# Kernel optimization log

Hardware: AMD Instinct MI355X
Metric: run time of the kernel (lower is better)

## Reference

```python
import jax, jax.numpy as jnp
import numpy as np

N = 50000          # total nodes (types: 20000/17000/13000)
E = 800000         # edges, avg degree 16
NUM_ETYPES = 6
ALPHA = 0.05       # residual-attention blend coefficient
SLOPE = 0.2        # leaky_relu negative slope


def _edge_softmax(e, dst, n):
    # softmax over incoming edges of each destination node; e: [E, H]
    m = jax.ops.segment_max(e, dst, num_segments=n)      # [N, H]
    ex = jnp.exp(e - m[dst])
    s = jax.ops.segment_sum(ex, dst, num_segments=n)     # [N, H]
    return ex / s[dst]


def _gat_layer(h, src, dst, etype, W, We, eemb, al, ar, ae, resW, res_attn, activate):
    n = h.shape[0]
    H, out = al.shape
    feat = (h @ W).reshape(n, H, out)                    # [N, H, out]
    T, edim = eemb.shape
    # edge-type attention term: embedding -> fc_e -> attn_e; only T distinct rows
    et_att = jnp.einsum('thd,hd->th', (eemb @ We).reshape(T, H, edim), ae)  # [T, H]
    el = jnp.einsum('nho,ho->nh', feat, al)              # [N, H]
    er = jnp.einsum('nho,ho->nh', feat, ar)              # [N, H]
    e = jax.nn.leaky_relu(el[src] + er[dst] + et_att[etype], SLOPE)  # [E, H]
    a = _edge_softmax(e, dst, n)                         # [E, H]
    if res_attn is not None:
        a = a * (1.0 - ALPHA) + res_attn * ALPHA
    rst = jax.ops.segment_sum(feat[src] * a[:, :, None], dst, num_segments=n)  # [N, H, out]
    if resW is not None:
        rst = rst + (h @ resW).reshape(n, H, out)
    if activate:
        rst = jax.nn.elu(rst)
    return rst, jax.lax.stop_gradient(a)


def _forward(x0, x1, x2, fcw0, fcb0, fcw1, fcb1, fcw2, fcb2,
             W0, We0, eemb0, al0, ar0, ae0,
             W1, We1, eemb1, al1, ar1, ae1, resW1,
             W2, We2, eemb2, al2, ar2, ae2, resW2,
             src, dst, etype):
    # per-type input projection then concat (feat_drop=0 -> identity)
    h = jnp.concatenate([x0 @ fcw0 + fcb0, x1 @ fcw1 + fcb1, x2 @ fcw2 + fcb2], axis=0)  # [N, 64]
    h1, a = _gat_layer(h, src, dst, etype, W0, We0, eemb0, al0, ar0, ae0, None, None, True)
    h1 = h1.reshape(h1.shape[0], -1)                     # [N, 256]
    h2, a = _gat_layer(h1, src, dst, etype, W1, We1, eemb1, al1, ar1, ae1, resW1, a, True)
    h2 = h2.reshape(h2.shape[0], -1)                     # [N, 256]
    logits, _ = _gat_layer(h2, src, dst, etype, W2, We2, eemb2, al2, ar2, ae2, resW2, None, False)
    return logits                                        # [N, 1, 16]


def setup_inputs():
    key = jax.random.key(0)
    ks = iter(jax.random.split(key, 48))
    def rn(shape, fan_in):
        return jax.random.normal(next(ks), shape, jnp.float32) / np.sqrt(fan_in)
    inp = {}
    inp['x0'] = jax.random.normal(next(ks), (20000, 128), jnp.float32)
    inp['x1'] = jax.random.normal(next(ks), (17000, 256), jnp.float32)
    inp['x2'] = jax.random.normal(next(ks), (13000, 64), jnp.float32)
    inp['fcw0'] = rn((128, 64), 128); inp['fcb0'] = jnp.zeros((64,), jnp.float32)
    inp['fcw1'] = rn((256, 64), 256); inp['fcb1'] = jnp.zeros((64,), jnp.float32)
    inp['fcw2'] = rn((64, 64), 64);   inp['fcb2'] = jnp.zeros((64,), jnp.float32)
    # layer 0: in=64 -> H=8, out=32
    inp['W0'] = rn((64, 256), 64); inp['We0'] = rn((64, 512), 64)
    inp['eemb0'] = rn((NUM_ETYPES, 64), 1.0)
    inp['al0'] = rn((8, 32), 32); inp['ar0'] = rn((8, 32), 32); inp['ae0'] = rn((8, 64), 64)
    # layer 1: in=256 -> H=8, out=32, residual
    inp['W1'] = rn((256, 256), 256); inp['We1'] = rn((64, 512), 64)
    inp['eemb1'] = rn((NUM_ETYPES, 64), 1.0)
    inp['al1'] = rn((8, 32), 32); inp['ar1'] = rn((8, 32), 32); inp['ae1'] = rn((8, 64), 64)
    inp['resW1'] = rn((256, 256), 256)
    # output layer: in=256 -> H=1, out=16, residual
    inp['W2'] = rn((256, 16), 256); inp['We2'] = rn((64, 64), 64)
    inp['eemb2'] = rn((NUM_ETYPES, 64), 1.0)
    inp['al2'] = rn((1, 16), 16); inp['ar2'] = rn((1, 16), 16); inp['ae2'] = rn((1, 64), 64)
    inp['resW2'] = rn((256, 16), 256)
    inp['src'] = jax.random.randint(next(ks), (E,), 0, N)
    inp['dst'] = jax.random.randint(next(ks), (E,), 0, N)
    inp['etype'] = jax.random.randint(next(ks), (E,), 0, NUM_ETYPES)
    return inp


def reference(x0, x1, x2, fcw0, fcb0, fcw1, fcb1, fcw2, fcb2,
              W0, We0, eemb0, al0, ar0, ae0,
              W1, We1, eemb1, al1, ar1, ae1, resW1,
              W2, We2, eemb2, al2, ar2, ae2, resW2,
              src, dst, etype):
    return _forward(x0, x1, x2, fcw0, fcb0, fcw1, fcb1, fcw2, fcb2,
                    W0, We0, eemb0, al0, ar0, ae0,
                    W1, We1, eemb1, al1, ar1, ae1, resW1,
                    W2, We2, eemb2, al2, ar2, ae2, resW2,
                    src, dst, etype)
```

## Files before the change

kernel.cpp:

```cpp
#include <hip/hip_runtime.h>
#include <hip/hip_bf16.h>

#define ALPHA 0.05f
#define SLOPE 0.2f
#define LCAP 128

typedef __attribute__((ext_vector_type(8))) short short8v;
typedef __attribute__((ext_vector_type(8))) unsigned short ushort8v;
typedef __attribute__((ext_vector_type(4))) float floatx4;

__device__ inline ushort f2b(float f) {
    uint u = __float_as_uint(f);
    return (ushort)((u + 0x7fffu + ((u >> 16) & 1u)) >> 16);
}
__device__ inline float b2f(ushort b) { return __uint_as_float(((uint)b) << 16); }

__device__ inline void gload_lds16(const ushort* g, ushort* l) {
    __builtin_amdgcn_global_load_lds(
        (const __attribute__((address_space(1))) uint*)g,
        (__attribute__((address_space(3))) uint*)l, 16, 0, 0);
}


__global__ void hist_kernel(const int* __restrict__ dst, int* __restrict__ counts, int E) {
    int e = blockIdx.x * blockDim.x + threadIdx.x;
    if (e < E) atomicAdd(&counts[dst[e]], 1);
}

__global__ __launch_bounds__(256) void scan_part(const int* __restrict__ counts,
                                                 int* __restrict__ offsets,
                                                 int* __restrict__ partial, int n) {
    __shared__ int sd[256];
    int i = blockIdx.x * 256 + threadIdx.x;
    int v = (i < n) ? counts[i] : 0;
    sd[threadIdx.x] = v;
    __syncthreads();
    for (int off = 1; off < 256; off <<= 1) {
        int t = (threadIdx.x >= off) ? sd[threadIdx.x - off] : 0;
        __syncthreads();
        sd[threadIdx.x] += t;
        __syncthreads();
    }
    if (i < n) offsets[i + 1] = sd[threadIdx.x];
    if (threadIdx.x == 255) partial[blockIdx.x] = sd[255];
}

__global__ __launch_bounds__(256) void scan_top(int* __restrict__ partial, int nb) {
    __shared__ int sd[256];
    int v = (threadIdx.x < nb) ? partial[threadIdx.x] : 0;
    sd[threadIdx.x] = v;
    __syncthreads();
    for (int off = 1; off < 256; off <<= 1) {
        int t = (threadIdx.x >= off) ? sd[threadIdx.x - off] : 0;
        __syncthreads();
        sd[threadIdx.x] += t;
        __syncthreads();
    }
    if (threadIdx.x < nb) partial[threadIdx.x] = sd[threadIdx.x];
}

__global__ __launch_bounds__(256) void scan_add(int* __restrict__ offsets,
                                                int* __restrict__ cursor,
                                                const int* __restrict__ partial, int n) {
    int i = blockIdx.x * 256 + threadIdx.x;
    if (i >= n) return;
    int add = (blockIdx.x > 0) ? partial[blockIdx.x - 1] : 0;
    int v = offsets[i + 1] + add;
    offsets[i + 1] = v;
    if (i + 1 < n) cursor[i + 1] = v;
    if (i == 0) { offsets[0] = 0; cursor[0] = 0; }
}

__global__ void scatter_kernel(const int* __restrict__ src, const int* __restrict__ dst,
                               const int* __restrict__ et, int* __restrict__ cursor,
                               int* __restrict__ se, int E) {
    int e = blockIdx.x * blockDim.x + threadIdx.x;
    if (e >= E) return;
    int d = dst[e];
    int pos = atomicAdd(&cursor[d], 1);
    se[pos] = (src[e] << 3) | et[e];
}


__global__ void wprep3(const float* __restrict__ W0f, const float* __restrict__ W1f,
                       const float* __restrict__ WRf, ushort* __restrict__ Wt0,
                       ushort* __restrict__ Wt1, ushort* __restrict__ WtR) {
    int i = blockIdx.x * blockDim.x + threadIdx.x;
    if (i < 16384) {
        int k = i / 256, n = i % 256;
        Wt0[n * 64 + k] = f2b(W0f[i]);
    } else if (i < 16384 + 65536) {
        int j = i - 16384;
        int k = j / 256, n = j % 256;
        Wt1[n * 256 + k] = f2b(W1f[j]);
    } else if (i < 16384 + 2 * 65536) {
        int j = i - 16384 - 65536;
        int k = j / 256, n = j % 256;
        WtR[n * 256 + k] = f2b(WRf[j]);
    }
}


__global__ __launch_bounds__(512) void etype_all(
    const float* __restrict__ eemb0, const float* __restrict__ We0, const float* __restrict__ ae0, float* __restrict__ out0,
    const float* __restrict__ eemb1, const float* __restrict__ We1, const float* __restrict__ ae1, float* __restrict__ out1,
    const float* __restrict__ eemb2, const float* __restrict__ We2, const float* __restrict__ ae2, float* __restrict__ out2) {
    int layer = blockIdx.x / 6, t = blockIdx.x % 6;
    const float *eemb, *We, *ae;
    float* out;
    int H;
    if (layer == 0)      { eemb = eemb0; We = We0; ae = ae0; out = out0; H = 8; }
    else if (layer == 1) { eemb = eemb1; We = We1; ae = ae1; out = out1; H = 8; }
    else                 { eemb = eemb2; We = We2; ae = ae2; out = out2; H = 1; }
    __shared__ float es[64];
    int j = threadIdx.x;
    if (j < 64) es[j] = eemb[t * 64 + j];
    __syncthreads();
    if (j >= H * 64) return;
    float wsum = 0.f;
#pragma unroll 8
    for (int k = 0; k < 64; ++k) wsum += es[k] * We[k * (H * 64) + j];
    float v = wsum * ae[j];
#pragma unroll
    for (int off = 32; off > 0; off >>= 1) v += __shfl_down(v, off, 64);
    if ((j & 63) == 0) out[t * H + (j >> 6)] = v;
}


template<bool ATTN>
__global__ __launch_bounds__(256) void gemm_bf16(const ushort* __restrict__ A,
                                                 const ushort* __restrict__ Bt,
                                                 ushort* __restrict__ Cb,
                                                 const float* __restrict__ al,
                                                 const float* __restrict__ ar,
                                                 float* __restrict__ el,
                                                 float* __restrict__ er,
                                                 int M, int N, int K) {
    __shared__ ushort As[128 * 32];
    __shared__ ushort Bs[128 * 32];
    int bm = blockIdx.y * 128, bn = blockIdx.x * 128;
    int tid = threadIdx.x;
    int wave = tid >> 6, lane = tid & 63;
    int wm = (wave >> 1) * 64, wn = (wave & 1) * 64;
    int r = tid >> 2, c = (tid & 3) * 8;
    floatx4 acc[4][4] = {};
    for (int k0 = 0; k0 < K; k0 += 32) {
        gload_lds16(&A[(long)(bm + r) * K + k0 + c],       &As[(size_t)tid * 8]);
        gload_lds16(&A[(long)(bm + 64 + r) * K + k0 + c],  &As[(size_t)(256 + tid) * 8]);
        gload_lds16(&Bt[(long)(bn + r) * K + k0 + c],      &Bs[(size_t)tid * 8]);
        gload_lds16(&Bt[(long)(bn + 64 + r) * K + k0 + c], &Bs[(size_t)(256 + tid) * 8]);
        __syncthreads();
        int lr = lane & 15, lk = (lane >> 4) * 8;
        short8v af[4], bfr[4];
#pragma unroll
        for (int i = 0; i < 4; ++i)
            af[i] = *reinterpret_cast<const short8v*>(&As[(wm + i * 16 + lr) * 32 + lk]);
#pragma unroll
        for (int j = 0; j < 4; ++j)
            bfr[j] = *reinterpret_cast<const short8v*>(&Bs[(wn + j * 16 + lr) * 32 + lk]);
#pragma unroll
        for (int i = 0; i < 4; ++i)
#pragma unroll
            for (int j = 0; j < 4; ++j)
                acc[i][j] = __builtin_amdgcn_mfma_f32_16x16x32_bf16(af[i], bfr[j], acc[i][j], 0, 0, 0);
        __syncthreads();
    }
    int col = lane & 15, rbase = (lane >> 4) * 4;
#pragma unroll
    for (int i = 0; i < 4; ++i) {
#pragma unroll
        for (int rr = 0; rr < 4; ++rr) {
            int gm = bm + wm + i * 16 + rbase + rr;
            if (gm >= M) continue;
#pragma unroll
            for (int j = 0; j < 4; ++j) {
                int gn = bn + wn + j * 16 + col;
                Cb[(long)gm * N + gn] = f2b(acc[i][j][rr]);
            }
        }
    }
    if (ATTN) {
        int hA = (bn + wn) >> 5;
        float alv[4], arv[4];
#pragma unroll
        for (int j = 0; j < 4; ++j) {
            int h = hA + (j >> 1);
            int o = (j & 1) * 16 + col;
            alv[j] = al[h * 32 + o];
            arv[j] = ar[h * 32 + o];
        }
#pragma unroll
        for (int i = 0; i < 4; ++i) {
#pragma unroll
            for (int rr = 0; rr < 4; ++rr) {
                float slA = acc[i][0][rr] * alv[0] + acc[i][1][rr] * alv[1];
                float slB = acc[i][2][rr] * alv[2] + acc[i][3][rr] * alv[3];
                float srA = acc[i][0][rr] * arv[0] + acc[i][1][rr] * arv[1];
                float srB = acc[i][2][rr] * arv[2] + acc[i][3][rr] * arv[3];
#pragma unroll
                for (int off = 1; off < 16; off <<= 1) {
                    slA += __shfl_xor(slA, off, 64);
                    slB += __shfl_xor(slB, off, 64);
                    srA += __shfl_xor(srA, off, 64);
                    srB += __shfl_xor(srB, off, 64);
                }
                int gm = bm + wm + i * 16 + rbase + rr;
                if (col == 0 && gm < M) {
                    el[gm * 8 + hA]     = slA;
                    el[gm * 8 + hA + 1] = slB;
                    er[gm * 8 + hA]     = srA;
                    er[gm * 8 + hA + 1] = srB;
                }
            }
        }
    }
}


__global__ __launch_bounds__(256) void gemm_dual(const ushort* __restrict__ A,
                                                 const ushort* __restrict__ B1,
                                                 const ushort* __restrict__ B2,
                                                 ushort* __restrict__ C1,
                                                 ushort* __restrict__ C2,
                                                 const float* __restrict__ al,
                                                 const float* __restrict__ ar,
                                                 float* __restrict__ el,
                                                 float* __restrict__ er,
                                                 int M, int N, int K) {
    __shared__ ushort As[128 * 32];
    __shared__ ushort Bs1[128 * 32];
    __shared__ ushort Bs2[128 * 32];
    int bm = blockIdx.y * 128, bn = blockIdx.x * 128;
    int tid = threadIdx.x;
    int wave = tid >> 6, lane = tid & 63;
    int wm = (wave >> 1) * 64, wn = (wave & 1) * 64;
    int r = tid >> 2, c = (tid & 3) * 8;
    floatx4 acc1[4][4] = {};
    floatx4 acc2[4][4] = {};
    for (int k0 = 0; k0 < K; k0 += 32) {
        gload_lds16(&A[(long)(bm + r) * K + k0 + c],        &As[(size_t)tid * 8]);
        gload_lds16(&A[(long)(bm + 64 + r) * K + k0 + c],   &As[(size_t)(256 + tid) * 8]);
        gload_lds16(&B1[(long)(bn + r) * K + k0 + c],       &Bs1[(size_t)tid * 8]);
        gload_lds16(&B1[(long)(bn + 64 + r) * K + k0 + c],  &Bs1[(size_t)(256 + tid) * 8]);
        gload_lds16(&B2[(long)(bn + r) * K + k0 + c],       &Bs2[(size_t)tid * 8]);
        gload_lds16(&B2[(long)(bn + 64 + r) * K + k0 + c],  &Bs2[(size_t)(256 + tid) * 8]);
        __syncthreads();
        int lr = lane & 15, lk = (lane >> 4) * 8;
        short8v af[4], bfr[4];
#pragma unroll
        for (int i = 0; i < 4; ++i)
            af[i] = *reinterpret_cast<const short8v*>(&As[(wm + i * 16 + lr) * 32 + lk]);
#pragma unroll
        for (int j = 0; j < 4; ++j)
            bfr[j] = *reinterpret_cast<const short8v*>(&Bs1[(wn + j * 16 + lr) * 32 + lk]);
#pragma unroll
        for (int i = 0; i < 4; ++i)
#pragma unroll
            for (int j = 0; j < 4; ++j)
                acc1[i][j] = __builtin_amdgcn_mfma_f32_16x16x32_bf16(af[i], bfr[j], acc1[i][j], 0, 0, 0);
#pragma unroll
        for (int j = 0; j < 4; ++j)
            bfr[j] = *reinterpret_cast<const short8v*>(&Bs2[(wn + j * 16 + lr) * 32 + lk]);
#pragma unroll
        for (int i = 0; i < 4; ++i)
#pragma unroll
            for (int j = 0; j < 4; ++j)
                acc2[i][j] = __builtin_amdgcn_mfma_f32_16x16x32_bf16(af[i], bfr[j], acc2[i][j], 0, 0, 0);
        __syncthreads();
    }
    int col = lane & 15, rbase = (lane >> 4) * 4;
#pragma unroll
    for (int i = 0; i < 4; ++i) {
#pragma unroll
        for (int rr = 0; rr < 4; ++rr) {
            int gm = bm + wm + i * 16 + rbase + rr;
            if (gm >= M) continue;
#pragma unroll
            for (int j = 0; j < 4; ++j) {
                int gn = bn + wn + j * 16 + col;
                C1[(long)gm * N + gn] = f2b(acc1[i][j][rr]);
                C2[(long)gm * N + gn] = f2b(acc2[i][j][rr]);
            }
        }
    }
    int hA = (bn + wn) >> 5;
    float alv[4], arv[4];
#pragma unroll
    for (int j = 0; j < 4; ++j) {
        int h = hA + (j >> 1);
        int o = (j & 1) * 16 + col;
        alv[j] = al[h * 32 + o];
        arv[j] = ar[h * 32 + o];
    }
#pragma unroll
    for (int i = 0; i < 4; ++i) {
#pragma unroll
        for (int rr = 0; rr < 4; ++rr) {
            float slA = acc1[i][0][rr] * alv[0] + acc1[i][1][rr] * alv[1];
            float slB = acc1[i][2][rr] * alv[2] + acc1[i][3][rr] * alv[3];
            float srA = acc1[i][0][rr] * arv[0] + acc1[i][1][rr] * arv[1];
            float srB = acc1[i][2][rr] * arv[2] + acc1[i][3][rr] * arv[3];
#pragma unroll
            for (int off = 1; off < 16; off <<= 1) {
                slA += __shfl_xor(slA, off, 64);
                slB += __shfl_xor(slB, off, 64);
                srA += __shfl_xor(srA, off, 64);
                srB += __shfl_xor(srB, off, 64);
            }
            int gm = bm + wm + i * 16 + rbase + rr;
            if (col == 0 && gm < M) {
                el[gm * 8 + hA]     = slA;
                el[gm * 8 + hA + 1] = slB;
                er[gm * 8 + hA]     = srA;
                er[gm * 8 + hA + 1] = srB;
            }
        }
    }
}


__global__ __launch_bounds__(256) void matmul64_fc3(
    const float* __restrict__ A0, const float* __restrict__ A1, const float* __restrict__ A2,
    const float* __restrict__ W0, const float* __restrict__ W1, const float* __restrict__ W2,
    const float* __restrict__ b0, const float* __restrict__ b1, const float* __restrict__ b2,
    ushort* __restrict__ C, int n0, int n1, int n2) {
    int z = blockIdx.z;
    const float *A, *W, *bias;
    int M, K;
    long coff;
    if (z == 0)      { A = A0; W = W0; bias = b0; M = n0; K = 128; coff = 0; }
    else if (z == 1) { A = A1; W = W1; bias = b1; M = n1; K = 256; coff = (long)n0 * 64; }
    else             { A = A2; W = W2; bias = b2; M = n2; K = 64;  coff = (long)(n0 + n1) * 64; }
    int bm = blockIdx.y * 64;
    if (bm >= M) return;
    __shared__ float As[16][68];
    __shared__ float Bs[16][68];
    int tx = threadIdx.x % 16, ty = threadIdx.x / 16;
    float acc[4][4] = {};
    for (int k0 = 0; k0 < K; k0 += 16) {
        for (int i = threadIdx.x; i < 64 * 16; i += 256) {
            int mm = i / 16, kk = i % 16;
            int gm = bm + mm;
            As[kk][mm] = (gm < M) ? A[(long)gm * K + k0 + kk] : 0.f;
        }
        for (int i = threadIdx.x; i < 16 * 64; i += 256) {
            int kk = i / 64, nn = i % 64;
            Bs[kk][nn] = W[(long)(k0 + kk) * 64 + nn];
        }
        __syncthreads();
#pragma unroll
        for (int kk = 0; kk < 16; ++kk) {
            float a[4], b[4];
#pragma unroll
            for (int i = 0; i < 4; ++i) a[i] = As[kk][ty * 4 + i];
#pragma unroll
            for (int j = 0; j < 4; ++j) b[j] = Bs[kk][tx * 4 + j];
#pragma unroll
            for (int i = 0; i < 4; ++i)
#pragma unroll
                for (int j = 0; j < 4; ++j) acc[i][j] += a[i] * b[j];
        }
        __syncthreads();
    }
#pragma unroll
    for (int i = 0; i < 4; ++i) {
        int gm = bm + ty * 4 + i;
        if (gm >= M) continue;
#pragma unroll
        for (int j = 0; j < 4; ++j) {
            int gn = tx * 4 + j;
            C[coff + (long)gm * 64 + gn] = f2b(acc[i][j] + bias[gn]);
        }
    }
}


__global__ __launch_bounds__(256) void matmul_n16_dual(const ushort* __restrict__ A,
                                                       const float* __restrict__ W2,
                                                       const float* __restrict__ WR,
                                                       ushort* __restrict__ feat2b,
                                                       float* __restrict__ resout,
                                                       const float* __restrict__ al,
                                                       const float* __restrict__ ar,
                                                       float* __restrict__ el,
                                                       float* __restrict__ er, int M) {
    __shared__ float Ws2[256 * 16];
    __shared__ float WsR[256 * 16];
    for (int i = threadIdx.x; i < 256 * 16; i += 256) {
        Ws2[i] = W2[i];
        WsR[i] = WR[i];
    }
    __syncthreads();
    int nn = threadIdx.x % 16;
    float alv = al[nn], arv = ar[nn];
#pragma unroll
    for (int rb = 0; rb < 2; ++rb) {
        int m = blockIdx.x * 32 + rb * 16 + threadIdx.x / 16;
        if (m >= M) continue;
        float s1 = 0.f, s2 = 0.f;
        for (int k8 = 0; k8 < 32; ++k8) {
            uint4 v = *reinterpret_cast<const uint4*>(&A[(long)m * 256 + k8 * 8]);
            const uint* vp = reinterpret_cast<const uint*>(&v);
#pragma unroll
            for (int q = 0; q < 4; ++q) {
                uint w2 = vp[q];
                float f0 = __uint_as_float((w2 & 0xffffu) << 16);
                float f1 = __uint_as_float(w2 & 0xffff0000u);
                int k = k8 * 8 + q * 2;
                s1 += f0 * Ws2[(k + 0) * 16 + nn] + f1 * Ws2[(k + 1) * 16 + nn];
                s2 += f0 * WsR[(k + 0) * 16 + nn] + f1 * WsR[(k + 1) * 16 + nn];
            }
        }
        feat2b[(long)m * 16 + nn] = f2b(s1);
        resout[(long)m * 16 + nn] = s2;
        float sl = s1 * alv, sr = s1 * arv;
#pragma unroll
        for (int off = 1; off < 16; off <<= 1) {
            sl += __shfl_xor(sl, off, 64);
            sr += __shfl_xor(sr, off, 64);
        }
        if (nn == 0) { el[m] = sl; er[m] = sr; }
    }
}


template<bool BLEND, bool SAVE, bool RES>
__global__ __launch_bounds__(64) void fused_edge_h8(
    const int* __restrict__ offsets, const int* __restrict__ se,
    const float* __restrict__ el, const float* __restrict__ er,
    const float* __restrict__ etatt,
    const ushort* __restrict__ featb,
    const ushort* __restrict__ a0_in, ushort* __restrict__ a0_out,
    const ushort* __restrict__ resin, ushort* __restrict__ outb, int N) {
    int d = blockIdx.x;
    int lane = threadIdx.x;
    int lo = offsets[d], hi = offsets[d + 1];
    int deg = hi - lo;
    __shared__ float a_lds[LCAP][8];
    __shared__ int   s_lds[LCAP];
    __shared__ float er_s[8];
    __shared__ float m_s[8], inv_s[8];
    if (lane < 8) er_s[lane] = er[d * 8 + lane];
    __syncthreads();
    bool fast = (deg <= LCAP);
    int half = lane >> 5, t = lane & 31;
    int h8 = t >> 2;
    uint4 pf[4];
    int npf = 0;
    if (fast) {
        for (int i = lane; i < deg * 8; i += 64) {
            int p = i >> 3, h = i & 7;
            int v0 = se[lo + p];
            int s = v0 >> 3, tt = v0 & 7;
            if (h == 0) s_lds[p] = s;
            float v = el[s * 8 + h] + er_s[h] + etatt[tt * 8 + h];
            a_lds[p][h] = v > 0.f ? v : SLOPE * v;
        }
        __syncthreads();
#pragma unroll
        for (int u = 0; u < 4; ++u) {
            int p = half + 2 * u;
            if (p < deg) {
                pf[u] = *reinterpret_cast<const uint4*>(&featb[(long)s_lds[p] * 256 + t * 8]);
                npf = u + 1;
            }
        }
        {
            int g = lane >> 3, h = lane & 7;
            float m = -INFINITY;
            for (int p = g; p < deg; p += 8) m = fmaxf(m, a_lds[p][h]);
#pragma unroll
            for (int off = 8; off < 64; off <<= 1) m = fmaxf(m, __shfl_xor(m, off, 64));
            float ssum = 0.f;
            for (int p = g; p < deg; p += 8) ssum += __expf(a_lds[p][h] - m);
#pragma unroll
            for (int off = 8; off < 64; off <<= 1) ssum += __shfl_xor(ssum, off, 64);
            if (g == 0) {
                m_s[h] = m;
                inv_s[h] = ssum > 0.f ? 1.f / ssum : 0.f;
            }
        }
        __syncthreads();
        for (int i = lane; i < deg * 8; i += 64) {
            int p = i >> 3, h = i & 7;
            float a = __expf(a_lds[p][h] - m_s[h]) * inv_s[h];
            if (BLEND) a = a * (1.f - ALPHA) + b2f(a0_in[lo * 8 + i]) * ALPHA;
            a_lds[p][h] = a;
            if (SAVE) a0_out[lo * 8 + i] = f2b(a);
        }
        __syncthreads();
    } else {
        int g = lane >> 3, h = lane & 7;
        float m = -INFINITY;
        for (int p = g; p < deg; p += 8) {
            int v0 = se[lo + p];
            int s = v0 >> 3, tt = v0 & 7;
            float v = el[s * 8 + h] + er_s[h] + etatt[tt * 8 + h];
            v = v > 0.f ? v : SLOPE * v;
            m = fmaxf(m, v);
        }
#pragma unroll
        for (int off = 8; off < 64; off <<= 1) m = fmaxf(m, __shfl_xor(m, off, 64));
        float ssum = 0.f;
        for (int p = g; p < deg; p += 8) {
            int v0 = se[lo + p];
            int s = v0 >> 3, tt = v0 & 7;
            float v = el[s * 8 + h] + er_s[h] + etatt[tt * 8 + h];
            v = v > 0.f ? v : SLOPE * v;
            ssum += __expf(v - m);
        }
#pragma unroll
        for (int off = 8; off < 64; off <<= 1) ssum += __shfl_xor(ssum, off, 64);
        if (g == 0) {
            m_s[h] = m;
            inv_s[h] = ssum > 0.f ? 1.f / ssum : 0.f;
        }
        __syncthreads();
        if (SAVE) {
            for (int i = lane; i < deg * 8; i += 64) {
                int p = i >> 3, hh = i & 7;
                int v0 = se[lo + p];
                int s = v0 >> 3, tt = v0 & 7;
                float v = el[s * 8 + hh] + er_s[hh] + etatt[tt * 8 + hh];
                v = v > 0.f ? v : SLOPE * v;
                float a = __expf(v - m_s[hh]) * inv_s[hh];
                if (BLEND) a = a * (1.f - ALPHA) + b2f(a0_in[lo * 8 + i]) * ALPHA;
                a0_out[lo * 8 + i] = f2b(a);
            }
        }
    }
    float acc[8];
#pragma unroll
    for (int k = 0; k < 8; ++k) acc[k] = 0.f;
    if (RES && half == 0) {
        uint4 rv = *reinterpret_cast<const uint4*>(&resin[(long)d * 256 + t * 8]);
        const uint* rp = reinterpret_cast<const uint*>(&rv);
#pragma unroll
        for (int q = 0; q < 4; ++q) {
            acc[2 * q]     = __uint_as_float(rp[q] << 16);
            acc[2 * q + 1] = __uint_as_float(rp[q] & 0xffff0000u);
        }
    }
    if (fast) {
#pragma unroll
        for (int u = 0; u < 4; ++u) {
            if (u < npf) {
                float a = a_lds[half + 2 * u][h8];
                const uint* fp = reinterpret_cast<const uint*>(&pf[u]);
#pragma unroll
                for (int q = 0; q < 4; ++q) {
                    acc[2 * q]     += __uint_as_float(fp[q] << 16) * a;
                    acc[2 * q + 1] += __uint_as_float(fp[q] & 0xffff0000u) * a;
                }
            }
        }
        int p = half + 8;
        for (; p + 6 < deg; p += 8) {
            int s0 = s_lds[p],     s1 = s_lds[p + 2];
            int s2 = s_lds[p + 4], s3 = s_lds[p + 6];
            float a0 = a_lds[p][h8],     a1 = a_lds[p + 2][h8];
            float a2 = a_lds[p + 4][h8], a3 = a_lds[p + 6][h8];
            uint4 f0 = *reinterpret_cast<const uint4*>(&featb[(long)s0 * 256 + t * 8]);
            uint4 f1 = *reinterpret_cast<const uint4*>(&featb[(long)s1 * 256 + t * 8]);
            uint4 f2 = *reinterpret_cast<const uint4*>(&featb[(long)s2 * 256 + t * 8]);
            uint4 f3 = *reinterpret_cast<const uint4*>(&featb[(long)s3 * 256 + t * 8]);
            const uint* q0 = reinterpret_cast<const uint*>(&f0);
            const uint* q1 = reinterpret_cast<const uint*>(&f1);
            const uint* q2 = reinterpret_cast<const uint*>(&f2);
            const uint* q3 = reinterpret_cast<const uint*>(&f3);
#pragma unroll
            for (int q = 0; q < 4; ++q) {
                acc[2 * q] += __uint_as_float(q0[q] << 16) * a0
                            + __uint_as_float(q1[q] << 16) * a1
                            + __uint_as_float(q2[q] << 16) * a2
                            + __uint_as_float(q3[q] << 16) * a3;
                acc[2 * q + 1] += __uint_as_float(q0[q] & 0xffff0000u) * a0
                                + __uint_as_float(q1[q] & 0xffff0000u) * a1
                                + __uint_as_float(q2[q] & 0xffff0000u) * a2
                                + __uint_as_float(q3[q] & 0xffff0000u) * a3;
            }
        }
        for (; p < deg; p += 2) {
            int s = s_lds[p];
            float a = a_lds[p][h8];
            uint4 fv = *reinterpret_cast<const uint4*>(&featb[(long)s * 256 + t * 8]);
            const uint* fp = reinterpret_cast<const uint*>(&fv);
#pragma unroll
            for (int q = 0; q < 4; ++q) {
                uint u = fp[q];
                acc[2 * q]     += __uint_as_float(u << 16) * a;
                acc[2 * q + 1] += __uint_as_float(u & 0xffff0000u) * a;
            }
        }
    } else {
        for (int p = half; p < deg; p += 2) {
            int v0 = se[lo + p];
            int s = v0 >> 3, tt = v0 & 7;
            float v = el[s * 8 + h8] + er_s[h8] + etatt[tt * 8 + h8];
            v = v > 0.f ? v : SLOPE * v;
            float a = __expf(v - m_s[h8]) * inv_s[h8];
            if (BLEND) a = a * (1.f - ALPHA) + b2f(a0_in[(long)(lo + p) * 8 + h8]) * ALPHA;
            uint4 fv = *reinterpret_cast<const uint4*>(&featb[(long)s * 256 + t * 8]);
            const uint* fp = reinterpret_cast<const uint*>(&fv);
#pragma unroll
            for (int q = 0; q < 4; ++q) {
                uint u = fp[q];
                acc[2 * q]     += __uint_as_float(u << 16) * a;
                acc[2 * q + 1] += __uint_as_float(u & 0xffff0000u) * a;
            }
        }
    }
#pragma unroll
    for (int k = 0; k < 8; ++k) acc[k] += __shfl_down(acc[k], 32);
    if (half == 0) {
        ushort8v o;
#pragma unroll
        for (int k = 0; k < 8; ++k) {
            float v = acc[k];
            v = v > 0.f ? v : __expf(v) - 1.f;
            o[k] = f2b(v);
        }
        *reinterpret_cast<ushort8v*>(&outb[(long)d * 256 + t * 8]) = o;
    }
}


__global__ __launch_bounds__(64) void fused_edge_h1(
    const int* __restrict__ offsets, const int* __restrict__ se,
    const float* __restrict__ el, const float* __restrict__ er,
    const float* __restrict__ etatt,
    const ushort* __restrict__ featb2, const float* __restrict__ resout,
    float* __restrict__ out, int N) {
    int d = blockIdx.x;
    int lane = threadIdx.x;
    int lo = offsets[d], hi = offsets[d + 1];
    int deg = hi - lo;
    __shared__ float a_lds[512];
    float er_d = er[d];
    bool fast = (deg <= 512);
    float m = -INFINITY, inv = 0.f;
    if (fast) {
        for (int i = lane; i < deg; i += 64) {
            int v0 = se[lo + i];
            int s = v0 >> 3, t = v0 & 7;
            float v = el[s] + er_d + etatt[t];
            a_lds[i] = v > 0.f ? v : SLOPE * v;
        }
        __syncthreads();
        for (int i = lane; i < deg; i += 64) m = fmaxf(m, a_lds[i]);
#pragma unroll
        for (int off = 1; off < 64; off <<= 1) m = fmaxf(m, __shfl_xor(m, off, 64));
        float ssum = 0.f;
        for (int i = lane; i < deg; i += 64) ssum += __expf(a_lds[i] - m);
#pragma unroll
        for (int off = 1; off < 64; off <<= 1) ssum += __shfl_xor(ssum, off, 64);
        inv = ssum > 0.f ? 1.f / ssum : 0.f;
        for (int i = lane; i < deg; i += 64) a_lds[i] = __expf(a_lds[i] - m) * inv;
        __syncthreads();
    } else {
        for (int i = lane; i < deg; i += 64) {
            int v0 = se[lo + i];
            int s = v0 >> 3, t = v0 & 7;
            float v = el[s] + er_d + etatt[t];
            v = v > 0.f ? v : SLOPE * v;
            m = fmaxf(m, v);
        }
#pragma unroll
        for (int off = 1; off < 64; off <<= 1) m = fmaxf(m, __shfl_xor(m, off, 64));
        float ssum = 0.f;
        for (int i = lane; i < deg; i += 64) {
            int v0 = se[lo + i];
            int s = v0 >> 3, t = v0 & 7;
            float v = el[s] + er_d + etatt[t];
            v = v > 0.f ? v : SLOPE * v;
            ssum += __expf(v - m);
        }
#pragma unroll
        for (int off = 1; off < 64; off <<= 1) ssum += __shfl_xor(ssum, off, 64);
        inv = ssum > 0.f ? 1.f / ssum : 0.f;
    }
    int g = lane >> 1, t = lane & 1;
    float acc[8];
#pragma unroll
    for (int k = 0; k < 8; ++k) acc[k] = 0.f;
    for (int p = g; p < deg; p += 32) {
        int v0 = se[lo + p];
        int s = v0 >> 3;
        float a;
        if (fast) a = a_lds[p];
        else {
            int tt = v0 & 7;
            float v = el[s] + er_d + etatt[tt];
            v = v > 0.f ? v : SLOPE * v;
            a = __expf(v - m) * inv;
        }
        uint4 fv = *reinterpret_cast<const uint4*>(&featb2[(long)s * 16 + t * 8]);
        const uint* fp = reinterpret_cast<const uint*>(&fv);
#pragma unroll
        for (int q = 0; q < 4; ++q) {
            acc[2 * q]     += __uint_as_float(fp[q] << 16) * a;
            acc[2 * q + 1] += __uint_as_float(fp[q] & 0xffff0000u) * a;
        }
    }
#pragma unroll
    for (int off = 2; off < 64; off <<= 1)
#pragma unroll
        for (int k = 0; k < 8; ++k) acc[k] += __shfl_down(acc[k], off);
    if (lane < 2) {
        const float* rp = &resout[(long)d * 16 + t * 8];
        float4 r0 = *reinterpret_cast<const float4*>(rp);
        float4 r1 = *reinterpret_cast<const float4*>(rp + 4);
        float* op = &out[(long)d * 16 + t * 8];
        *reinterpret_cast<float4*>(op)     = make_float4(acc[0] + r0.x, acc[1] + r0.y, acc[2] + r0.z, acc[3] + r0.w);
        *reinterpret_cast<float4*>(op + 4) = make_float4(acc[4] + r1.x, acc[5] + r1.y, acc[6] + r1.z, acc[7] + r1.w);
    }
}


extern "C" void kernel_launch(void* const* d_in, const int* in_sizes, int n_in,
                              void* d_out, int out_size, void* d_ws, size_t ws_size,
                              hipStream_t stream) {
    const float* x0   = (const float*)d_in[0];
    const float* x1   = (const float*)d_in[1];
    const float* x2   = (const float*)d_in[2];
    const float* fcw0 = (const float*)d_in[3];
    const float* fcb0 = (const float*)d_in[4];
    const float* fcw1 = (const float*)d_in[5];
    const float* fcb1 = (const float*)d_in[6];
    const float* fcw2 = (const float*)d_in[7];
    const float* fcb2 = (const float*)d_in[8];
    const float* W0   = (const float*)d_in[9];
    const float* We0  = (const float*)d_in[10];
    const float* eemb0= (const float*)d_in[11];
    const float* al0  = (const float*)d_in[12];
    const float* ar0  = (const float*)d_in[13];
    const float* ae0  = (const float*)d_in[14];
    const float* W1   = (const float*)d_in[15];
    const float* We1  = (const float*)d_in[16];
    const float* eemb1= (const float*)d_in[17];
    const float* al1  = (const float*)d_in[18];
    const float* ar1  = (const float*)d_in[19];
    const float* ae1  = (const float*)d_in[20];
    const float* resW1= (const float*)d_in[21];
    const float* W2   = (const float*)d_in[22];
    const float* We2  = (const float*)d_in[23];
    const float* eemb2= (const float*)d_in[24];
    const float* al2  = (const float*)d_in[25];
    const float* ar2  = (const float*)d_in[26];
    const float* ae2  = (const float*)d_in[27];
    const float* resW2= (const float*)d_in[28];
    const int* src    = (const int*)d_in[29];
    const int* dst    = (const int*)d_in[30];
    const int* etype  = (const int*)d_in[31];

    const int n0 = in_sizes[0] / 128;
    const int n1 = in_sizes[1] / 256;
    const int n2 = in_sizes[2] / 64;
    const int N  = n0 + n1 + n2;
    const int E  = in_sizes[29];

    char* w = (char*)d_ws;
    auto alloc = [&](size_t bytes) {
        char* p = w;
        w += (bytes + 255) & ~(size_t)255;
        return p;
    };
    int*    counts  = (int*)alloc((size_t)N * 4);
    int*    offsets = (int*)alloc((size_t)(N + 1) * 4);
    int*    cursor  = (int*)alloc((size_t)N * 4);
    int*    partial = (int*)alloc(1024 * 4);
    int*    se      = (int*)alloc((size_t)E * 4);
    ushort* h2res   = (ushort*)alloc((size_t)N * 256 * 2);
    ushort* a0b     = (ushort*)alloc((size_t)E * 8 * 2);
    ushort* h0bf    = (ushort*)alloc((size_t)N * 64 * 2 + 128 * 256 * 2);
    ushort* featb   = (ushort*)alloc((size_t)N * 256 * 2);
    ushort* h1bf    = (ushort*)alloc((size_t)N * 256 * 2 + 128 * 256 * 2);
    ushort* h2bf    = (ushort*)alloc((size_t)N * 256 * 2);
    float*  el      = (float*)alloc((size_t)N * 8 * 4);
    float*  er      = (float*)alloc((size_t)N * 8 * 4);
    float*  etatt0  = (float*)alloc(64 * 4);
    float*  etatt1  = (float*)alloc(64 * 4);
    float*  etatt2  = (float*)alloc(64 * 4);
    ushort* Wt0     = (ushort*)alloc((size_t)256 * 64 * 2);
    ushort* Wt1     = (ushort*)alloc((size_t)256 * 256 * 2);
    ushort* WtR     = (ushort*)alloc((size_t)256 * 256 * 2);
    ushort* feat2b  = (ushort*)alloc((size_t)N * 16 * 2);
    float*  resout  = (float*)alloc((size_t)N * 16 * 4);
    float*  out     = (float*)d_out;

    const int TB = 256;
    int eb = (E + TB - 1) / TB;
    int nb1 = (N + 255) / 256;

    hipMemsetAsync(counts, 0, (size_t)N * 4, stream);
    hist_kernel<<<eb, TB, 0, stream>>>(dst, counts, E);
    scan_part<<<nb1, 256, 0, stream>>>(counts, offsets, partial, N);
    scan_top<<<1, 256, 0, stream>>>(partial, nb1);
    scan_add<<<nb1, 256, 0, stream>>>(offsets, cursor, partial, N);
    scatter_kernel<<<eb, TB, 0, stream>>>(src, dst, etype, cursor, se, E);

    wprep3<<<(16384 + 2 * 65536 + TB - 1) / TB, TB, 0, stream>>>(W0, W1, resW1, Wt0, Wt1, WtR);
    etype_all<<<18, 512, 0, stream>>>(eemb0, We0, ae0, etatt0,
                                      eemb1, We1, ae1, etatt1,
                                      eemb2, We2, ae2, etatt2);

    {
        int maxTiles = (n0 + 63) / 64;
        int t1 = (n1 + 63) / 64, t2 = (n2 + 63) / 64;
        if (t1 > maxTiles) maxTiles = t1;
        if (t2 > maxTiles) maxTiles = t2;
        dim3 g(1, maxTiles, 3);
        matmul64_fc3<<<g, TB, 0, stream>>>(x0, x1, x2, fcw0, fcw1, fcw2,
                                           fcb0, fcb1, fcb2, h0bf, n0, n1, n2);
    }

    dim3 gg(256 / 128, (N + 127) / 128);

    gemm_bf16<true><<<gg, TB, 0, stream>>>(h0bf, Wt0, featb, al0, ar0, el, er, N, 256, 64);
    fused_edge_h8<false, true, false><<<N, 64, 0, stream>>>(
        offsets, se, el, er, etatt0, featb, nullptr, a0b, nullptr, h1bf, N);

    gemm_dual<<<gg, TB, 0, stream>>>(h1bf, Wt1, WtR, featb, h2res, al1, ar1, el, er, N, 256, 256);
    fused_edge_h8<true, false, true><<<N, 64, 0, stream>>>(
        offsets, se, el, er, etatt1, featb, a0b, nullptr, h2res, h2bf, N);

    matmul_n16_dual<<<(N + 31) / 32, TB, 0, stream>>>(
        h2bf, W2, resW2, feat2b, resout, al2, ar2, el, er, N);
    fused_edge_h1<<<N, 64, 0, stream>>>(offsets, se, el, er, etatt2, feat2b, resout, out, N);
}
```

Baseline: 441.6 us.

## Replace FP32 input-projection matmul with bf16 MFMA GEMM over pre-converted inputs

After: 419.1 us. -5.1%, faster.

```diff
diff --git a/kernel.cpp b/kernel.cpp
--- a/kernel.cpp
+++ b/kernel.cpp
@@ -82,9 +82,14 @@
 }
 
 
-__global__ void wprep3(const float* __restrict__ W0f, const float* __restrict__ W1f,
-                       const float* __restrict__ WRf, ushort* __restrict__ Wt0,
-                       ushort* __restrict__ Wt1, ushort* __restrict__ WtR) {
+__global__ void wprep(const float* __restrict__ W0f, const float* __restrict__ W1f,
+                      const float* __restrict__ WRf,
+                      const float* __restrict__ fw0, const float* __restrict__ fw1,
+                      const float* __restrict__ fw2,
+                      ushort* __restrict__ Wt0, ushort* __restrict__ Wt1,
+                      ushort* __restrict__ WtR,
+                      ushort* __restrict__ ft0, ushort* __restrict__ ft1,
+                      ushort* __restrict__ ft2) {
     int i = blockIdx.x * blockDim.x + threadIdx.x;
     if (i < 16384) {
         int k = i / 256, n = i % 256;
@@ -97,7 +102,33 @@
         int j = i - 16384 - 65536;
         int k = j / 256, n = j % 256;
         WtR[n * 256 + k] = f2b(WRf[j]);
-    }
+    } else if (i < 147456 + 8192) {
+        int j = i - 147456;
+        int k = j / 64, n = j % 64;
+        ft0[n * 128 + k] = f2b(fw0[j]);
+    } else if (i < 147456 + 8192 + 16384) {
+        int j = i - 147456 - 8192;
+        int k = j / 64, n = j % 64;
+        ft1[n * 256 + k] = f2b(fw1[j]);
+    } else if (i < 147456 + 8192 + 16384 + 4096) {
+        int j = i - 147456 - 8192 - 16384;
+        int k = j / 64, n = j % 64;
+        ft2[n * 64 + k] = f2b(fw2[j]);
+    }
+}
+
+
+__global__ void xprep(const float* __restrict__ x0, const float* __restrict__ x1,
+                      const float* __restrict__ x2, ushort* __restrict__ xb,
+                      long t0, long t1, long t2) {
+    long i = (long)blockIdx.x * blockDim.x + threadIdx.x;
+    float4 v;
+    if (i < t0) v = reinterpret_cast<const float4*>(x0)[i];
+    else if (i < t0 + t1) v = reinterpret_cast<const float4*>(x1)[i - t0];
+    else if (i < t0 + t1 + t2) v = reinterpret_cast<const float4*>(x2)[i - t0 - t1];
+    else return;
+    ushort4 u = {f2b(v.x), f2b(v.y), f2b(v.z), f2b(v.w)};
+    reinterpret_cast<ushort4*>(xb)[i] = u;
 }
 
 
@@ -319,57 +350,64 @@
 }
 
 
-__global__ __launch_bounds__(256) void matmul64_fc3(
-    const float* __restrict__ A0, const float* __restrict__ A1, const float* __restrict__ A2,
-    const float* __restrict__ W0, const float* __restrict__ W1, const float* __restrict__ W2,
-    const float* __restrict__ b0, const float* __restrict__ b1, const float* __restrict__ b2,
-    ushort* __restrict__ C, int n0, int n1, int n2) {
+__global__ __launch_bounds__(256) void gemm_fc(const ushort* __restrict__ xb,
+                                               const ushort* __restrict__ ft0,
+                                               const ushort* __restrict__ ft1,
+                                               const ushort* __restrict__ ft2,
+                                               const float* __restrict__ b0,
+                                               const float* __restrict__ b1,
+                                               const float* __restrict__ b2,
+                                               ushort* __restrict__ C,
+                                               int n0, int n1, int n2) {
     int z = blockIdx.z;
-    const float *A, *W, *bias;
+    const ushort *A, *Bt;
+    const float* bias;
     int M, K;
     long coff;
-    if (z == 0)      { A = A0; W = W0; bias = b0; M = n0; K = 128; coff = 0; }
-    else if (z == 1) { A = A1; W = W1; bias = b1; M = n1; K = 256; coff = (long)n0 * 64; }
-    else             { A = A2; W = W2; bias = b2; M = n2; K = 64;  coff = (long)(n0 + n1) * 64; }
-    int bm = blockIdx.y * 64;
+    if (z == 0)      { A = xb; Bt = ft0; bias = b0; M = n0; K = 128; coff = 0; }
+    else if (z == 1) { A = xb + (long)n0 * 128; Bt = ft1; bias = b1; M = n1; K = 256; coff = (long)n0 * 64; }
+    else             { A = xb + (long)n0 * 128 + (long)n1 * 256; Bt = ft2; bias = b2; M = n2; K = 64; coff = (long)(n0 + n1) * 64; }
+    int bm = blockIdx.y * 128;
     if (bm >= M) return;
-    __shared__ float As[16][68];
-    __shared__ float Bs[16][68];
-    int tx = threadIdx.x % 16, ty = threadIdx.x / 16;
-    float acc[4][4] = {};
-    for (int k0 = 0; k0 < K; k0 += 16) {
-        for (int i = threadIdx.x; i < 64 * 16; i += 256) {
-            int mm = i / 16, kk = i % 16;
-            int gm = bm + mm;
-            As[kk][mm] = (gm < M) ? A[(long)gm * K + k0 + kk] : 0.f;
-        }
-        for (int i = threadIdx.x; i < 16 * 64; i += 256) {
-            int kk = i / 64, nn = i % 64;
-            Bs[kk][nn] = W[(long)(k0 + kk) * 64 + nn];
-        }
-        __syncthreads();
-#pragma unroll
-        for (int kk = 0; kk < 16; ++kk) {
-            float a[4], b[4];
-#pragma unroll
-            for (int i = 0; i < 4; ++i) a[i] = As[kk][ty * 4 + i];
-#pragma unroll
-            for (int j = 0; j < 4; ++j) b[j] = Bs[kk][tx * 4 + j];
-#pragma unroll
-            for (int i = 0; i < 4; ++i)
-#pragma unroll
-                for (int j = 0; j < 4; ++j) acc[i][j] += a[i] * b[j];
-        }
-        __syncthreads();
-    }
+    __shared__ ushort As[128 * 32];
+    __shared__ ushort Bs[64 * 32];
+    int tid = threadIdx.x;
+    int wave = tid >> 6, lane = tid & 63;
+    int wm = (wave >> 1) * 64, wn = (wave & 1) * 32;
+    int r = tid >> 2, c = (tid & 3) * 8;
+    floatx4 acc[4][2] = {};
+    for (int k0 = 0; k0 < K; k0 += 32) {
+        gload_lds16(&A[(long)(bm + r) * K + k0 + c],      &As[(size_t)tid * 8]);
+        gload_lds16(&A[(long)(bm + 64 + r) * K + k0 + c], &As[(size_t)(256 + tid) * 8]);
+        gload_lds16(&Bt[(long)r * K + k0 + c],            &Bs[(size_t)tid * 8]);
+        __syncthreads();
+        int lr = lane & 15, lk = (lane >> 4) * 8;
+        short8v af[4], bfr[2];
+#pragma unroll
+        for (int i = 0; i < 4; ++i)
+            af[i] = *reinterpret_cast<const short8v*>(&As[(wm + i * 16 + lr) * 32 + lk]);
+#pragma unroll
+        for (int j = 0; j < 2; ++j)
+            bfr[j] = *reinterpret_cast<const short8v*>(&Bs[(wn + j * 16 + lr) * 32 + lk]);
+#pragma unroll
+        for (int i = 0; i < 4; ++i)
+#pragma unroll
+            for (int j = 0; j < 2; ++j)
+                acc[i][j] = __builtin_amdgcn_mfma_f32_16x16x32_bf16(af[i], bfr[j], acc[i][j], 0, 0, 0);
+        __syncthreads();
+    }
+    int col = lane & 15, rbase = (lane >> 4) * 4;
 #pragma unroll
     for (int i = 0; i < 4; ++i) {
-        int gm = bm + ty * 4 + i;
-        if (gm >= M) continue;
-#pragma unroll
-        for (int j = 0; j < 4; ++j) {
-            int gn = tx * 4 + j;
-            C[coff + (long)gm * 64 + gn] = f2b(acc[i][j] + bias[gn]);
+#pragma unroll
+        for (int rr = 0; rr < 4; ++rr) {
+            int gm = bm + wm + i * 16 + rbase + rr;
+            if (gm >= M) continue;
+#pragma unroll
+            for (int j = 0; j < 2; ++j) {
+                int gn = wn + j * 16 + col;
+                C[coff + (long)gm * 64 + gn] = f2b(acc[i][j][rr] + bias[gn]);
+            }
         }
     }
 }
@@ -758,6 +796,7 @@
     const int n2 = in_sizes[2] / 64;
     const int N  = n0 + n1 + n2;
     const int E  = in_sizes[29];
+    const long s0 = in_sizes[0], s1 = in_sizes[1], s2 = in_sizes[2];
 
     char* w = (char*)d_ws;
     auto alloc = [&](size_t bytes) {
@@ -772,6 +811,7 @@
     int*    se      = (int*)alloc((size_t)E * 4);
     ushort* h2res   = (ushort*)alloc((size_t)N * 256 * 2);
     ushort* a0b     = (ushort*)alloc((size_t)E * 8 * 2);
+    ushort* xb      = (ushort*)alloc((size_t)(s0 + s1 + s2) * 2 + 128 * 256 * 2);
     ushort* h0bf    = (ushort*)alloc((size_t)N * 64 * 2 + 128 * 256 * 2);
     ushort* featb   = (ushort*)alloc((size_t)N * 256 * 2);
     ushort* h1bf    = (ushort*)alloc((size_t)N * 256 * 2 + 128 * 256 * 2);
@@ -784,6 +824,9 @@
     ushort* Wt0     = (ushort*)alloc((size_t)256 * 64 * 2);
     ushort* Wt1     = (ushort*)alloc((size_t)256 * 256 * 2);
     ushort* WtR     = (ushort*)alloc((size_t)256 * 256 * 2);
+    ushort* ft0     = (ushort*)alloc((size_t)64 * 128 * 2);
+    ushort* ft1     = (ushort*)alloc((size_t)64 * 256 * 2);
+    ushort* ft2     = (ushort*)alloc((size_t)64 * 64 * 2);
     ushort* feat2b  = (ushort*)alloc((size_t)N * 16 * 2);
     float*  resout  = (float*)alloc((size_t)N * 16 * 4);
     float*  out     = (float*)d_out;
@@ -799,19 +842,19 @@
     scan_add<<<nb1, 256, 0, stream>>>(offsets, cursor, partial, N);
     scatter_kernel<<<eb, TB, 0, stream>>>(src, dst, etype, cursor, se, E);
 
-    wprep3<<<(16384 + 2 * 65536 + TB - 1) / TB, TB, 0, stream>>>(W0, W1, resW1, Wt0, Wt1, WtR);
+    wprep<<<(176128 + TB - 1) / TB, TB, 0, stream>>>(W0, W1, resW1, fcw0, fcw1, fcw2,
+                                                     Wt0, Wt1, WtR, ft0, ft1, ft2);
     etype_all<<<18, 512, 0, stream>>>(eemb0, We0, ae0, etatt0,
                                       eemb1, We1, ae1, etatt1,
                                       eemb2, We2, ae2, etatt2);
+    long tot4 = (s0 + s1 + s2) / 4;
+    xprep<<<(int)((tot4 + TB - 1) / TB), TB, 0, stream>>>(x0, x1, x2, xb, s0 / 4, s1 / 4, s2 / 4);
 
     {
-        int maxTiles = (n0 + 63) / 64;
-        int t1 = (n1 + 63) / 64, t2 = (n2 + 63) / 64;
-        if (t1 > maxTiles) maxTiles = t1;
-        if (t2 > maxTiles) maxTiles = t2;
-        dim3 g(1, maxTiles, 3);
-        matmul64_fc3<<<g, TB, 0, stream>>>(x0, x1, x2, fcw0, fcw1, fcw2,
-                                           fcb0, fcb1, fcb2, h0bf, n0, n1, n2);
+        int maxM = n0 > n1 ? n0 : n1;
+        if (n2 > maxM) maxM = n2;
+        dim3 g(1, (maxM + 127) / 128, 3);
+        gemm_fc<<<g, TB, 0, stream>>>(xb, ft0, ft1, ft2, fcb0, fcb1, fcb2, h0bf, n0, n1, n2);
     }
 
     dim3 gg(256 / 128, (N + 127) / 128);
```
